# Optimization experiments

Hardware: AMD Instinct MI355X
Metric: run time of the kernel (lower is better)

## Reference

```python
import jax, jax.numpy as jnp
import numpy as np

B, D, N, K = 16, 128, 16384, 64


def setup_inputs() -> dict:
    key = jax.random.key(0)
    k1, k2, k3, k4 = jax.random.split(key, 4)
    x = jax.random.normal(k1, (B, D, N), dtype=jnp.float32)
    mu = jax.random.normal(k2, (K, D), dtype=jnp.float32)
    log_sigma = 0.1 * jax.random.normal(k3, (K, D), dtype=jnp.float32)
    log_alpha = 0.1 * jax.random.normal(k4, (K,), dtype=jnp.float32)
    return {"x": x, "mu": mu, "log_sigma": log_sigma, "log_alpha": log_alpha}


def reference(x, mu, log_sigma, log_alpha):
    # x: (B, D, N) -> (B, N, D)
    xt = jnp.transpose(x, (0, 2, 1))
    # F.normalize(mu): L2-normalize each cluster center along D (eps=1e-12)
    mu_n = mu / jnp.maximum(jnp.linalg.norm(mu, axis=1, keepdims=True), 1e-12)
    sigma_inv = jnp.exp(-log_sigma)                     # (K, D)
    log_sigma_sum = jnp.sum(log_sigma, axis=1)          # (K,)
    # dist_{bnk} = sum_d (x-mu)^2 * sinv, decomposed into GEMMs
    xsq_term = jnp.einsum('bnd,kd->bnk', xt * xt, sigma_inv)
    cross = jnp.einsum('bnd,kd->bnk', xt, mu_n * sigma_inv)
    mu_term = jnp.sum(mu_n * mu_n * sigma_inv, axis=1)  # (K,)
    dist = xsq_term - 2.0 * cross + mu_term
    logits = -dist + log_alpha - 0.5 * log_sigma_sum    # (B, N, K)
    posterior = jax.nn.softmax(logits, axis=-1)
    return jnp.transpose(posterior, (0, 2, 1))          # (B, K, N)
```

## Files before the change

### kernel.cpp

```cpp
#include <hip/hip_runtime.h>
#include <hip/hip_bf16.h>

#define LOG2E 1.4426950408889634f

constexpr int Dn = 128;
constexpr int Nn = 16384;
constexpr int Kn = 64;
constexpr int Bn = 16;

typedef float f32x4 __attribute__((ext_vector_type(4)));
typedef unsigned int u32x4 __attribute__((ext_vector_type(4)));
typedef short short8 __attribute__((ext_vector_type(8)));

__device__ __forceinline__ unsigned int rnhi(float f) {
    unsigned int u = __float_as_uint(f);
    return (u + 0x7FFFu + ((u >> 16) & 1u)) & 0xFFFF0000u;
}

__global__ __launch_bounds__(64) void gmm_prep(const float* __restrict__ mu,
                                               const float* __restrict__ log_sigma,
                                               const float* __restrict__ log_alpha,
                                               unsigned short* __restrict__ wfrag,
                                               float* __restrict__ cout) {
    const int k = blockIdx.x;
    const int l = threadIdx.x;
    const int d0 = 2 * l;
    float m0 = mu[k * Dn + d0];
    float m1 = mu[k * Dn + d0 + 1];
    float s0 = log_sigma[k * Dn + d0];
    float s1 = log_sigma[k * Dn + d0 + 1];
    float nrm2 = m0 * m0 + m1 * m1;
    float lss = s0 + s1;
    #pragma unroll
    for (int off = 32; off > 0; off >>= 1) {
        nrm2 += __shfl_xor(nrm2, off);
        lss  += __shfl_xor(lss, off);
    }
    const float inv_nrm = 1.0f / fmaxf(sqrtf(nrm2), 1e-12f);
    const float mn0 = m0 * inv_nrm, mn1 = m1 * inv_nrm;
    const float si0 = expf(-s0), si1 = expf(-s1);
    float mt = mn0 * mn0 * si0 + mn1 * mn1 * si1;
    #pragma unroll
    for (int off = 32; off > 0; off >>= 1) mt += __shfl_xor(mt, off);

    const float av[2] = {-si0 * LOG2E, -si1 * LOG2E};
    const float bv[2] = {2.0f * mn0 * si0 * LOG2E, 2.0f * mn1 * si1 * LOG2E};
    const int ks = k >> 4;
    #pragma unroll
    for (int dd = 0; dd < 2; ++dd) {
        const int d = d0 + dd;
        const unsigned int ah = rnhi(av[dd]);
        const unsigned int al = rnhi(av[dd] - __uint_as_float(ah));
        const unsigned int bh = rnhi(bv[dd]);
        const unsigned int bl = rnhi(bv[dd] - __uint_as_float(bh));
        const int s = d >> 5, h = (d >> 3) & 3, j = d & 7;
        const int lane = (h << 4) | (k & 15);
        const size_t base = ((size_t)((ks * 4 + s) * 4) * 64 + lane) * 8 + j;
        wfrag[base + 0 * 64 * 8] = (unsigned short)(ah >> 16);
        wfrag[base + 1 * 64 * 8] = (unsigned short)(al >> 16);
        wfrag[base + 2 * 64 * 8] = (unsigned short)(bh >> 16);
        wfrag[base + 3 * 64 * 8] = (unsigned short)(bl >> 16);
    }
    if (l == 0) cout[k] = (log_alpha[k] - 0.5f * lss - mt) * LOG2E;
}

__device__ __forceinline__ unsigned int pk2(float a, float b) {
    __hip_bfloat162 h = __float22bfloat162_rn(make_float2(a, b));
    unsigned int u;
    __builtin_memcpy(&u, &h, 4);
    return u;
}

__global__ __launch_bounds__(512)
__attribute__((amdgpu_waves_per_eu(4, 4)))
void gmm_main(const float* __restrict__ x,
              const unsigned short* __restrict__ wf,
              const float* __restrict__ cks,
              float* __restrict__ out) {
    __shared__ unsigned short sF[2][4][8][64][8];
    __shared__ float sRedM[4][128];
    __shared__ float sRedS[4][128];

    const int tid = threadIdx.x;
    const int l = tid & 63;
    const int wid = __builtin_amdgcn_readfirstlane(tid >> 6);
    const int ks = wid & 3;
    const int tp = wid >> 2;
    const int h = l >> 4;
    const int col = l & 15;
    const int b = blockIdx.y;
    const int nwin = blockIdx.x * 128;
    const float* xwin = x + (size_t)b * Dn * Nn + nwin;

    const int stok = tid & 127;
    const int sdg = tid >> 7;
    const int stt = stok >> 4;
    const int slane = (sdg << 4) | (stok & 15);
    const float* sx = xwin + stok + (size_t)(sdg * 8) * Nn;

    f32x4 acc[4];
    #pragma unroll
    for (int tt = 0; tt < 4; ++tt)
        #pragma unroll
        for (int r = 0; r < 4; ++r)
            acc[tt][r] = cks[ks * 16 + h * 4 + r];

    auto cvtwrite = [&](int buf, const float* xv) {
        u32x4 Xh, Xl, Th, Tl;
        #pragma unroll
        for (int p = 0; p < 4; ++p) {
            const float x0 = xv[2 * p], x1 = xv[2 * p + 1];
            const float t0 = x0 * x0, t1 = x1 * x1;
            const unsigned int xh = pk2(x0, x1);
            Xh[p] = xh;
            Xl[p] = pk2(x0 - __uint_as_float(xh << 16),
                        x1 - __uint_as_float(xh & 0xFFFF0000u));
            const unsigned int th = pk2(t0, t1);
            Th[p] = th;
            Tl[p] = pk2(t0 - __uint_as_float(th << 16),
                        t1 - __uint_as_float(th & 0xFFFF0000u));
        }
        *(u32x4*)&sF[buf][0][stt][slane][0] = Xh;
        *(u32x4*)&sF[buf][1][stt][slane][0] = Xl;
        *(u32x4*)&sF[buf][2][stt][slane][0] = Th;
        *(u32x4*)&sF[buf][3][stt][slane][0] = Tl;
    };

    {
        float xr[8];
        #pragma unroll
        for (int j = 0; j < 8; ++j) xr[j] = sx[(size_t)j * Nn];
        cvtwrite(0, xr);
    }
    __syncthreads();

#define BC(v) __builtin_bit_cast(short8, v)
    #pragma unroll
    for (int s = 0; s < 4; ++s) {
        float xn[8];
        if (s < 3) {
            #pragma unroll
            for (int j = 0; j < 8; ++j)
                xn[j] = sx[(size_t)((s + 1) * 32 + j) * Nn];
        }

        u32x4 Ws[4];
        #pragma unroll
        for (int m = 0; m < 4; ++m)
            Ws[m] = *(const u32x4*)(wf +
                     ((size_t)((ks * 4 + s) * 4 + m) * 64 + l) * 8);

        #pragma unroll
        for (int tt = 0; tt < 4; ++tt) {
            const int ttg = tp * 4 + tt;
            const u32x4 Xh = *(const u32x4*)&sF[s & 1][0][ttg][l][0];
            const u32x4 Xl = *(const u32x4*)&sF[s & 1][1][ttg][l][0];
            const u32x4 Th = *(const u32x4*)&sF[s & 1][2][ttg][l][0];
            const u32x4 Tl = *(const u32x4*)&sF[s & 1][3][ttg][l][0];
            acc[tt] = __builtin_amdgcn_mfma_f32_16x16x32_bf16(
                          BC(Ws[0]), BC(Th), acc[tt], 0, 0, 0);
            acc[tt] = __builtin_amdgcn_mfma_f32_16x16x32_bf16(
                          BC(Ws[1]), BC(Th), acc[tt], 0, 0, 0);
            acc[tt] = __builtin_amdgcn_mfma_f32_16x16x32_bf16(
                          BC(Ws[0]), BC(Tl), acc[tt], 0, 0, 0);
            acc[tt] = __builtin_amdgcn_mfma_f32_16x16x32_bf16(
                          BC(Ws[2]), BC(Xh), acc[tt], 0, 0, 0);
            acc[tt] = __builtin_amdgcn_mfma_f32_16x16x32_bf16(
                          BC(Ws[3]), BC(Xh), acc[tt], 0, 0, 0);
            acc[tt] = __builtin_amdgcn_mfma_f32_16x16x32_bf16(
                          BC(Ws[2]), BC(Xl), acc[tt], 0, 0, 0);
        }

        if (s < 3) {
            cvtwrite((s + 1) & 1, xn);
            __syncthreads();
        }
    }
#undef BC

    #pragma unroll
    for (int tt = 0; tt < 4; ++tt) {
        float m = fmaxf(fmaxf(acc[tt][0], acc[tt][1]),
                        fmaxf(acc[tt][2], acc[tt][3]));
        m = fmaxf(m, __shfl_xor(m, 16));
        m = fmaxf(m, __shfl_xor(m, 32));
        if (l < 16) sRedM[ks][tp * 64 + tt * 16 + l] = m;
    }
    __syncthreads();
    float stot[4];
    #pragma unroll
    for (int tt = 0; tt < 4; ++tt) {
        const int idx = tp * 64 + tt * 16 + col;
        float m = sRedM[0][idx];
        m = fmaxf(m, sRedM[1][idx]);
        m = fmaxf(m, sRedM[2][idx]);
        m = fmaxf(m, sRedM[3][idx]);
        float ssum = 0.f;
        #pragma unroll
        for (int r = 0; r < 4; ++r) {
            acc[tt][r] = __builtin_amdgcn_exp2f(acc[tt][r] - m);
            ssum += acc[tt][r];
        }
        ssum += __shfl_xor(ssum, 16);
        ssum += __shfl_xor(ssum, 32);
        if (l < 16) sRedS[ks][tp * 64 + tt * 16 + l] = ssum;
    }
    __syncthreads();
    #pragma unroll
    for (int tt = 0; tt < 4; ++tt) {
        const int idx = tp * 64 + tt * 16 + col;
        stot[tt] = sRedS[0][idx] + sRedS[1][idx] + sRedS[2][idx] + sRedS[3][idx];
    }

    #pragma unroll
    for (int tt = 0; tt < 4; ++tt) {
        const float inv = 1.0f / stot[tt];
        float* op = out + ((size_t)(b * Kn + ks * 16 + h * 4)) * Nn +
                    nwin + tp * 64 + tt * 16 + col;
        #pragma unroll
        for (int r = 0; r < 4; ++r) {
            *op = acc[tt][r] * inv;
            op += Nn;
        }
    }
}

extern "C" void kernel_launch(void* const* d_in, const int* in_sizes, int n_in,
                              void* d_out, int out_size, void* d_ws, size_t ws_size,
                              hipStream_t stream) {
    const float* x  = (const float*)d_in[0];
    const float* mu = (const float*)d_in[1];
    const float* ls = (const float*)d_in[2];
    const float* la = (const float*)d_in[3];
    float* out = (float*)d_out;

    unsigned short* wbuf = (unsigned short*)d_ws;
    float* cbuf = (float*)((char*)d_ws + 65536);

    gmm_prep<<<dim3(Kn), dim3(64), 0, stream>>>(mu, ls, la, wbuf, cbuf);
    gmm_main<<<dim3(Nn / 128, Bn), dim3(512), 0, stream>>>(x, wbuf, cbuf, out);
}
```

Before: 221.9 us.

## Retile waves to 2x2 K-by-token blocks and prefetch x two stages ahead

Each wave now computes two K-slices by two token tiles instead of one K-slice by four token tiles. Each LDS fragment it loads is therefore reused across two weight sets, which halves LDS reads per MFMA, while global weight-fragment loads per wave double. The cross-wave softmax reduction now needs only two partials per token. Global x loads are prefetched two stages ahead (p1/p2) to hide latency better, at the cost of extra registers.

```diff
diff --git a/kernel.cpp b/kernel.cpp
--- a/kernel.cpp
+++ b/kernel.cpp
@@ -78,14 +78,14 @@
               const float* __restrict__ cks,
               float* __restrict__ out) {
     __shared__ unsigned short sF[2][4][8][64][8];
-    __shared__ float sRedM[4][128];
-    __shared__ float sRedS[4][128];
+    __shared__ float sRedM[2][128];
+    __shared__ float sRedS[2][128];
 
     const int tid = threadIdx.x;
     const int l = tid & 63;
     const int wid = __builtin_amdgcn_readfirstlane(tid >> 6);
-    const int ks = wid & 3;
-    const int tp = wid >> 2;
+    const int ks2 = wid & 1;
+    const int tq = wid >> 1;
     const int h = l >> 4;
     const int col = l & 15;
     const int b = blockIdx.y;
@@ -98,12 +98,14 @@
     const int slane = (sdg << 4) | (stok & 15);
     const float* sx = xwin + stok + (size_t)(sdg * 8) * Nn;
 
-    f32x4 acc[4];
-    #pragma unroll
-    for (int tt = 0; tt < 4; ++tt)
-        #pragma unroll
-        for (int r = 0; r < 4; ++r)
-            acc[tt][r] = cks[ks * 16 + h * 4 + r];
+    f32x4 acc[2][2];
+    #pragma unroll
+    for (int st = 0; st < 2; ++st)
+        #pragma unroll
+        for (int tile = 0; tile < 2; ++tile)
+            #pragma unroll
+            for (int r = 0; r < 4; ++r)
+                acc[st][tile][r] = cks[(2 * ks2 + st) * 16 + h * 4 + r];
 
     auto cvtwrite = [&](int buf, const float* xv) {
         u32x4 Xh, Xl, Th, Tl;
@@ -126,101 +128,116 @@
         *(u32x4*)&sF[buf][3][stt][slane][0] = Tl;
     };
 
+    float p1[8];
     {
         float xr[8];
         #pragma unroll
         for (int j = 0; j < 8; ++j) xr[j] = sx[(size_t)j * Nn];
         cvtwrite(0, xr);
     }
+    #pragma unroll
+    for (int j = 0; j < 8; ++j) p1[j] = sx[(size_t)(32 + j) * Nn];
     __syncthreads();
 
 #define BC(v) __builtin_bit_cast(short8, v)
     #pragma unroll
     for (int s = 0; s < 4; ++s) {
-        float xn[8];
+        float p2[8];
+        if (s < 2) {
+            #pragma unroll
+            for (int j = 0; j < 8; ++j)
+                p2[j] = sx[(size_t)((s + 2) * 32 + j) * Nn];
+        }
+
+        u32x4 Ws[2][4];
+        #pragma unroll
+        for (int st = 0; st < 2; ++st)
+            #pragma unroll
+            for (int m = 0; m < 4; ++m)
+                Ws[st][m] = *(const u32x4*)(wf +
+                    ((size_t)(((2 * ks2 + st) * 4 + s) * 4 + m) * 64 + l) * 8);
+
+        #pragma unroll
+        for (int tile = 0; tile < 2; ++tile) {
+            const int gtile = 2 * tq + tile;
+            const u32x4 Xh = *(const u32x4*)&sF[s & 1][0][gtile][l][0];
+            const u32x4 Xl = *(const u32x4*)&sF[s & 1][1][gtile][l][0];
+            const u32x4 Th = *(const u32x4*)&sF[s & 1][2][gtile][l][0];
+            const u32x4 Tl = *(const u32x4*)&sF[s & 1][3][gtile][l][0];
+            #pragma unroll
+            for (int st = 0; st < 2; ++st) {
+                acc[st][tile] = __builtin_amdgcn_mfma_f32_16x16x32_bf16(
+                    BC(Ws[st][0]), BC(Th), acc[st][tile], 0, 0, 0);
+                acc[st][tile] = __builtin_amdgcn_mfma_f32_16x16x32_bf16(
+                    BC(Ws[st][1]), BC(Th), acc[st][tile], 0, 0, 0);
+                acc[st][tile] = __builtin_amdgcn_mfma_f32_16x16x32_bf16(
+                    BC(Ws[st][0]), BC(Tl), acc[st][tile], 0, 0, 0);
+                acc[st][tile] = __builtin_amdgcn_mfma_f32_16x16x32_bf16(
+                    BC(Ws[st][2]), BC(Xh), acc[st][tile], 0, 0, 0);
+                acc[st][tile] = __builtin_amdgcn_mfma_f32_16x16x32_bf16(
+                    BC(Ws[st][3]), BC(Xh), acc[st][tile], 0, 0, 0);
+                acc[st][tile] = __builtin_amdgcn_mfma_f32_16x16x32_bf16(
+                    BC(Ws[st][2]), BC(Xl), acc[st][tile], 0, 0, 0);
+            }
+        }
+
         if (s < 3) {
-            #pragma unroll
-            for (int j = 0; j < 8; ++j)
-                xn[j] = sx[(size_t)((s + 1) * 32 + j) * Nn];
-        }
-
-        u32x4 Ws[4];
-        #pragma unroll
-        for (int m = 0; m < 4; ++m)
-            Ws[m] = *(const u32x4*)(wf +
-                     ((size_t)((ks * 4 + s) * 4 + m) * 64 + l) * 8);
-
-        #pragma unroll
-        for (int tt = 0; tt < 4; ++tt) {
-            const int ttg = tp * 4 + tt;
-            const u32x4 Xh = *(const u32x4*)&sF[s & 1][0][ttg][l][0];
-            const u32x4 Xl = *(const u32x4*)&sF[s & 1][1][ttg][l][0];
-            const u32x4 Th = *(const u32x4*)&sF[s & 1][2][ttg][l][0];
-            const u32x4 Tl = *(const u32x4*)&sF[s & 1][3][ttg][l][0];
-            acc[tt] = __builtin_amdgcn_mfma_f32_16x16x32_bf16(
-                          BC(Ws[0]), BC(Th), acc[tt], 0, 0, 0);
-            acc[tt] = __builtin_amdgcn_mfma_f32_16x16x32_bf16(
-                          BC(Ws[1]), BC(Th), acc[tt], 0, 0, 0);
-            acc[tt] = __builtin_amdgcn_mfma_f32_16x16x32_bf16(
-                          BC(Ws[0]), BC(Tl), acc[tt], 0, 0, 0);
-            acc[tt] = __builtin_amdgcn_mfma_f32_16x16x32_bf16(
-                          BC(Ws[2]), BC(Xh), acc[tt], 0, 0, 0);
-            acc[tt] = __builtin_amdgcn_mfma_f32_16x16x32_bf16(
-                          BC(Ws[3]), BC(Xh), acc[tt], 0, 0, 0);
-            acc[tt] = __builtin_amdgcn_mfma_f32_16x16x32_bf16(
-                          BC(Ws[2]), BC(Xl), acc[tt], 0, 0, 0);
-        }
-
-        if (s < 3) {
-            cvtwrite((s + 1) & 1, xn);
+            cvtwrite((s + 1) & 1, p1);
+            #pragma unroll
+            for (int j = 0; j < 8; ++j) p1[j] = p2[j];
             __syncthreads();
         }
     }
 #undef BC
 
     #pragma unroll
-    for (int tt = 0; tt < 4; ++tt) {
-        float m = fmaxf(fmaxf(acc[tt][0], acc[tt][1]),
-                        fmaxf(acc[tt][2], acc[tt][3]));
+    for (int tile = 0; tile < 2; ++tile) {
+        const int gtile = 2 * tq + tile;
+        float m = fmaxf(fmaxf(acc[0][tile][0], acc[0][tile][1]),
+                        fmaxf(acc[0][tile][2], acc[0][tile][3]));
+        m = fmaxf(m, fmaxf(fmaxf(acc[1][tile][0], acc[1][tile][1]),
+                           fmaxf(acc[1][tile][2], acc[1][tile][3])));
         m = fmaxf(m, __shfl_xor(m, 16));
         m = fmaxf(m, __shfl_xor(m, 32));
-        if (l < 16) sRedM[ks][tp * 64 + tt * 16 + l] = m;
+        if (l < 16) sRedM[ks2][gtile * 16 + l] = m;
     }
     __syncthreads();
-    float stot[4];
-    #pragma unroll
-    for (int tt = 0; tt < 4; ++tt) {
-        const int idx = tp * 64 + tt * 16 + col;
-        float m = sRedM[0][idx];
-        m = fmaxf(m, sRedM[1][idx]);
-        m = fmaxf(m, sRedM[2][idx]);
-        m = fmaxf(m, sRedM[3][idx]);
+    float stot[2];
+    #pragma unroll
+    for (int tile = 0; tile < 2; ++tile) {
+        const int idx = (2 * tq + tile) * 16 + col;
+        const float m = fmaxf(sRedM[0][idx], sRedM[1][idx]);
         float ssum = 0.f;
         #pragma unroll
-        for (int r = 0; r < 4; ++r) {
-            acc[tt][r] = __builtin_amdgcn_exp2f(acc[tt][r] - m);
-            ssum += acc[tt][r];
-        }
+        for (int st = 0; st < 2; ++st)
+            #pragma unroll
+            for (int r = 0; r < 4; ++r) {
+                acc[st][tile][r] = __builtin_amdgcn_exp2f(acc[st][tile][r] - m);
+                ssum += acc[st][tile][r];
+            }
         ssum += __shfl_xor(ssum, 16);
         ssum += __shfl_xor(ssum, 32);
-        if (l < 16) sRedS[ks][tp * 64 + tt * 16 + l] = ssum;
+        if (l < 16) sRedS[ks2][(2 * tq + tile) * 16 + l] = ssum;
     }
     __syncthreads();
     #pragma unroll
-    for (int tt = 0; tt < 4; ++tt) {
-        const int idx = tp * 64 + tt * 16 + col;
-        stot[tt] = sRedS[0][idx] + sRedS[1][idx] + sRedS[2][idx] + sRedS[3][idx];
-    }
-
-    #pragma unroll
-    for (int tt = 0; tt < 4; ++tt) {
-        const float inv = 1.0f / stot[tt];
-        float* op = out + ((size_t)(b * Kn + ks * 16 + h * 4)) * Nn +
-                    nwin + tp * 64 + tt * 16 + col;
-        #pragma unroll
-        for (int r = 0; r < 4; ++r) {
-            *op = acc[tt][r] * inv;
-            op += Nn;
+    for (int tile = 0; tile < 2; ++tile) {
+        const int idx = (2 * tq + tile) * 16 + col;
+        stot[tile] = sRedS[0][idx] + sRedS[1][idx];
+    }
+
+    #pragma unroll
+    for (int tile = 0; tile < 2; ++tile) {
+        const float inv = 1.0f / stot[tile];
+        #pragma unroll
+        for (int st = 0; st < 2; ++st) {
+            float* op = out + ((size_t)(b * Kn + (2 * ks2 + st) * 16 + h * 4)) * Nn +
+                        nwin + (2 * tq + tile) * 16 + col;
+            #pragma unroll
+            for (int r = 0; r < 4; ++r) {
+                *op = acc[st][tile][r] * inv;
+                op += Nn;
+            }
         }
     }
 }
```

Result: no change. 225.3 us (+1.5%).

## Single-buffer LDS staging and raise waves-per-EU target to eight

Applied to the files above, without the earlier changes.

Drops the double-buffered LDS staging to a single buffer, which halves shared memory, and restructures the loop to sync before and after each convert/write. It also raises the waves-per-EU hint from 4 to 8 so more blocks can be co-resident and hide global-load latency. The cost is an extra barrier per stage and no overlap between the LDS write and the MFMA reads. The tighter register budget at 8 waves may cause spills given the 16 accumulator floats plus fragment registers.

```diff
diff --git a/kernel.cpp b/kernel.cpp
--- a/kernel.cpp
+++ b/kernel.cpp
@@ -72,12 +72,12 @@
 }
 
 __global__ __launch_bounds__(512)
-__attribute__((amdgpu_waves_per_eu(4, 4)))
+__attribute__((amdgpu_waves_per_eu(8, 8)))
 void gmm_main(const float* __restrict__ x,
               const unsigned short* __restrict__ wf,
               const float* __restrict__ cks,
               float* __restrict__ out) {
-    __shared__ unsigned short sF[2][4][8][64][8];
+    __shared__ unsigned short sF[4][8][64][8];
     __shared__ float sRedM[4][128];
     __shared__ float sRedS[4][128];
 
@@ -105,7 +105,7 @@
         for (int r = 0; r < 4; ++r)
             acc[tt][r] = cks[ks * 16 + h * 4 + r];
 
-    auto cvtwrite = [&](int buf, const float* xv) {
+    auto cvtwrite = [&](const float* xv) {
         u32x4 Xh, Xl, Th, Tl;
         #pragma unroll
         for (int p = 0; p < 4; ++p) {
@@ -120,29 +120,29 @@
             Tl[p] = pk2(t0 - __uint_as_float(th << 16),
                         t1 - __uint_as_float(th & 0xFFFF0000u));
         }
-        *(u32x4*)&sF[buf][0][stt][slane][0] = Xh;
-        *(u32x4*)&sF[buf][1][stt][slane][0] = Xl;
-        *(u32x4*)&sF[buf][2][stt][slane][0] = Th;
-        *(u32x4*)&sF[buf][3][stt][slane][0] = Tl;
+        *(u32x4*)&sF[0][stt][slane][0] = Xh;
+        *(u32x4*)&sF[1][stt][slane][0] = Xl;
+        *(u32x4*)&sF[2][stt][slane][0] = Th;
+        *(u32x4*)&sF[3][stt][slane][0] = Tl;
     };
 
-    {
-        float xr[8];
-        #pragma unroll
-        for (int j = 0; j < 8; ++j) xr[j] = sx[(size_t)j * Nn];
-        cvtwrite(0, xr);
-    }
-    __syncthreads();
+    float xr[8];
+    #pragma unroll
+    for (int j = 0; j < 8; ++j) xr[j] = sx[(size_t)j * Nn];
 
 #define BC(v) __builtin_bit_cast(short8, v)
     #pragma unroll
     for (int s = 0; s < 4; ++s) {
+        if (s > 0) __syncthreads();
+        cvtwrite(xr);
+
         float xn[8];
         if (s < 3) {
             #pragma unroll
             for (int j = 0; j < 8; ++j)
                 xn[j] = sx[(size_t)((s + 1) * 32 + j) * Nn];
         }
+        __syncthreads();
 
         u32x4 Ws[4];
         #pragma unroll
@@ -152,11 +152,11 @@
 
         #pragma unroll
         for (int tt = 0; tt < 4; ++tt) {
-            const int ttg = tp * 4 + tt;
-            const u32x4 Xh = *(const u32x4*)&sF[s & 1][0][ttg][l][0];
-            const u32x4 Xl = *(const u32x4*)&sF[s & 1][1][ttg][l][0];
-            const u32x4 Th = *(const u32x4*)&sF[s & 1][2][ttg][l][0];
-            const u32x4 Tl = *(const u32x4*)&sF[s & 1][3][ttg][l][0];
+            const int gtile = 4 * tp + tt;
+            const u32x4 Xh = *(const u32x4*)&sF[0][gtile][l][0];
+            const u32x4 Xl = *(const u32x4*)&sF[1][gtile][l][0];
+            const u32x4 Th = *(const u32x4*)&sF[2][gtile][l][0];
+            const u32x4 Tl = *(const u32x4*)&sF[3][gtile][l][0];
             acc[tt] = __builtin_amdgcn_mfma_f32_16x16x32_bf16(
                           BC(Ws[0]), BC(Th), acc[tt], 0, 0, 0);
             acc[tt] = __builtin_amdgcn_mfma_f32_16x16x32_bf16(
@@ -171,13 +171,12 @@
                           BC(Ws[2]), BC(Xl), acc[tt], 0, 0, 0);
         }
 
-        if (s < 3) {
-            cvtwrite((s + 1) & 1, xn);
-            __syncthreads();
-        }
+        #pragma unroll
+        for (int j = 0; j < 8; ++j) xr[j] = xn[j];
     }
 #undef BC
 
+    __syncthreads();
     #pragma unroll
     for (int tt = 0; tt < 4; ++tt) {
         float m = fmaxf(fmaxf(acc[tt][0], acc[tt][1]),
@@ -216,7 +215,7 @@
     for (int tt = 0; tt < 4; ++tt) {
         const float inv = 1.0f / stot[tt];
         float* op = out + ((size_t)(b * Kn + ks * 16 + h * 4)) * Nn +
-                    nwin + tp * 64 + tt * 16 + col;
+                    nwin + (4 * tp + tt) * 16 + col;
         #pragma unroll
         for (int r = 0; r < 4; ++r) {
             *op = acc[tt][r] * inv;
```

Measured after the change: 225.1 us. Within noise of the previous version (+1.4%).
